# Kernel tuning notes

Hardware: AMD Instinct MI355X
Metric: run time of the kernel (lower is better)

Reference implementation:

```python
import jax, jax.numpy as jnp
import numpy as np

H, D, DIM = 8, 128, 1024   # heads, dim_head, model dim (inner_dim = H*D = DIM)
QB, N = 16, 512            # 'q' and 'n' dims of the [q, n, dim] inputs


def layer_norm(x, g, b, eps=1e-5):
    mu = x.mean(-1, keepdims=True)
    var = ((x - mu) ** 2).mean(-1, keepdims=True)
    return (x - mu) / jnp.sqrt(var + eps) * g + b


def setup_inputs() -> dict:
    key = jax.random.key(0)
    ks = jax.random.split(key, 8)
    rn = lambda k, shape, s=1.0: jax.random.normal(k, shape, jnp.float32) * s
    return {
        'q': rn(ks[0], (QB, N, DIM)),
        'k': rn(ks[1], (QB, N, DIM)),
        'v': rn(ks[2], (QB, N, DIM)),
        'ln_g': jnp.ones(DIM, jnp.float32),
        'ln_b': jnp.zeros(DIM, jnp.float32),
        'w_in': rn(ks[3], (H * D, DIM), 0.02),          # Linear(dim -> inner_dim), no bias
        'wp_w1': rn(ks[4], (D, 2 * D), 0.05),           # weight_predictor Linear(2d -> d)
        'wp_b1': jnp.zeros(D, jnp.float32),
        'wp_ln_g': jnp.ones(D, jnp.float32),
        'wp_ln_b': jnp.zeros(D, jnp.float32),
        'wp_w2': rn(ks[5], (3, D), 0.05),               # Linear(d -> 3)
        'wp_b2': jnp.zeros(3, jnp.float32),
        'w_out': rn(ks[6], (DIM, H * D), 0.02),         # output Linear(inner_dim -> dim)
        'b_out': jnp.zeros(DIM, jnp.float32),
    }


def reference(q, k, v, ln_g, ln_b, w_in, wp_w1, wp_b1, wp_ln_g, wp_ln_b,
              wp_w2, wp_b2, w_out, b_out):
    def proj(t):
        x = layer_norm(t, ln_g, ln_b) @ w_in.T                 # [Q, N, H*D]
        Qd, Nd = t.shape[0], t.shape[1]
        return x.reshape(Qd, Nd, H, D).transpose(2, 0, 1, 3)   # [h, q, n, d]

    f_q, f_k, f_v = proj(q), proj(k), proj(v)

    # cosine similarity component
    dots = jnp.einsum('hqnd,hqmd->hqnm', f_q, f_k)
    qn = jnp.linalg.norm(f_q, axis=-1)                          # [h, q, n]
    kn = jnp.linalg.norm(f_k, axis=-1)                          # [h, q, m]
    cosine_sim = dots / (qn[..., :, None] * kn[..., None, :])

    q_centered = f_q - f_q.mean(-1, keepdims=True)

    # variance component (unbiased variance, clipped ratio vs target_var=1)
    q_var = jnp.var(f_q, axis=-1, ddof=1)
    k_var = jnp.var(f_k, axis=-1, ddof=1)
    q_ratio = 2.0 * jnp.minimum(q_var, 1.0) / (q_var + 1.0)
    k_ratio = 2.0 * jnp.minimum(k_var, 1.0) / (k_var + 1.0)
    var_component = jnp.einsum('hqn,hqm->hqnm', q_ratio, k_ratio)

    # decorrelation-scaled covariance component (overwrites the dead loop in the source)
    q_flat = q_centered.reshape(H, -1, D)                        # [h, q*n, d]
    feat_corr = jnp.einsum('hnd,hne->hde', q_flat, q_flat) / q_flat.shape[1]
    feat_corr = feat_corr * (1.0 - jnp.eye(D, dtype=feat_corr.dtype))
    decorr_score = jnp.linalg.norm(feat_corr, axis=(-2, -1)) / (D * D)
    decorr_scale = jnp.exp(-5.0 * decorr_score)[:, None, None, None]
    cov_component = cosine_sim * decorr_scale

    # dynamic per-head weight mixing
    q_global = f_q.mean(axis=(1, 2))                             # [h, d]
    k_global = f_k.mean(axis=(1, 2))
    feats = jnp.concatenate([q_global, k_global], axis=-1)       # [h, 2d]
    h1 = jnp.maximum(layer_norm(feats @ wp_w1.T + wp_b1, wp_ln_g, wp_ln_b), 0.0)
    weights = jax.nn.softmax(h1 @ wp_w2.T + wp_b2, axis=-1)      # [h, 3]
    cw = weights[:, 0][:, None, None, None]
    vw = weights[:, 1][:, None, None, None]
    ww = weights[:, 2][:, None, None, None]
    mixed = cw * cosine_sim + vw * cov_component + ww * var_component

    out = jnp.einsum('hqnm,hqmd->hqnd', mixed, f_v)
    out = out.transpose(1, 2, 0, 3).reshape(q.shape[0], q.shape[1], H * D)
    return out @ w_out.T + b_out
```

## Files before the change

### kernel.cpp

```cpp
#include <hip/hip_runtime.h>
#include <hip/hip_bf16.h>

typedef unsigned short u16;
typedef __attribute__((ext_vector_type(8))) short short8;
typedef __attribute__((ext_vector_type(4))) float floatx4;

#define H 8
#define D 128
#define DIM 1024
#define QB 16
#define NSEQ 512
#define R 8192

__device__ inline u16 f2b(float x) {
    union { float f; unsigned int u; } c{x};
    unsigned int lsb = (c.u >> 16) & 1;
    unsigned int r = c.u + 0x7fffu + lsb;
    return (u16)(r >> 16);
}
__device__ inline float b2f(u16 u) {
    union { unsigned int i; float f; } c;
    c.i = (unsigned int)u << 16;
    return c.f;
}

#define GLOAD_LDS16(gptr, lptr)                                                        \
    __builtin_amdgcn_global_load_lds(                                                  \
        (const __attribute__((address_space(1))) unsigned int*)(gptr),                 \
        (__attribute__((address_space(3))) unsigned int*)(lptr), 16, 0, 0)

__global__ __launch_bounds__(256) void ln_all(const float* __restrict__ q,
                                              const float* __restrict__ k,
                                              const float* __restrict__ v,
                                              const float* __restrict__ g,
                                              const float* __restrict__ b,
                                              u16* __restrict__ out) {
    const float* src = (blockIdx.y == 0) ? q : (blockIdx.y == 1) ? k : v;
    int r = blockIdx.x;
    int tid = threadIdx.x;
    const int wv = tid >> 6, lane = tid & 63;
    const float* row = src + (size_t)r * DIM;
    float4 vv = *(const float4*)(row + tid * 4);
    float sum = vv.x + vv.y + vv.z + vv.w;
    float sq = vv.x * vv.x + vv.y * vv.y + vv.z * vv.z + vv.w * vv.w;
#pragma unroll
    for (int o = 32; o > 0; o >>= 1) {
        sum += __shfl_xor(sum, o);
        sq  += __shfl_xor(sq, o);
    }
    __shared__ float s1[4], s2[4];
    if (lane == 0) { s1[wv] = sum; s2[wv] = sq; }
    __syncthreads();
    sum = s1[0] + s1[1] + s1[2] + s1[3];
    sq  = s2[0] + s2[1] + s2[2] + s2[3];
    float mean = sum * (1.0f / DIM);
    float var = sq * (1.0f / DIM) - mean * mean;
    float rstd = rsqrtf(var + 1e-5f);
    float4 gv = *(const float4*)(g + tid * 4);
    float4 bv = *(const float4*)(b + tid * 4);
    ushort4 pk;
    pk.x = f2b((vv.x - mean) * rstd * gv.x + bv.x);
    pk.y = f2b((vv.y - mean) * rstd * gv.y + bv.y);
    pk.z = f2b((vv.z - mean) * rstd * gv.z + bv.z);
    pk.w = f2b((vv.w - mean) * rstd * gv.w + bv.w);
    *(ushort4*)(out + ((size_t)blockIdx.y * R + r) * DIM + tid * 4) = pk;
}

__global__ __launch_bounds__(256) void cvt2_kernel(const float* __restrict__ a,
                                                   const float* __restrict__ b,
                                                   u16* __restrict__ oa,
                                                   u16* __restrict__ ob, int n4each) {
    int i = blockIdx.x * 256 + threadIdx.x;
    const float* src; u16* dst; int j;
    if (i < n4each) { src = a; dst = oa; j = i; }
    else            { src = b; dst = ob; j = i - n4each; }
    float4 v = *(const float4*)(src + (size_t)j * 4);
    ushort4 pk;
    pk.x = f2b(v.x); pk.y = f2b(v.y); pk.z = f2b(v.z); pk.w = f2b(v.w);
    *(ushort4*)(dst + (size_t)j * 4) = pk;
}

__global__ __launch_bounds__(256) void gemm_qkv(const u16* __restrict__ A,
                                                const u16* __restrict__ B,
                                                u16* __restrict__ qT,
                                                u16* __restrict__ fqb,
                                                u16* __restrict__ kTh,
                                                u16* __restrict__ vT,
                                                float* __restrict__ qn,
                                                float* __restrict__ qm,
                                                float* __restrict__ qr,
                                                float* __restrict__ kn,
                                                float* __restrict__ kr) {
    __shared__ u16 smem[19712];
    u16* As  = smem;
    u16* Bs  = smem + 4096;
    u16* As2 = smem + 8192;
    u16* Bs2 = smem + 12288;
    float* sred = (float*)(smem + 18432);
    float* invb = (float*)(smem + 19456);

    const int tid = threadIdx.x;
    const int bb = blockIdx.x;
    const int xcd = bb & 7, j0 = bb >> 3;
    const int h = j0 & 7;
    const int rowblk = xcd * 24 + (j0 >> 3);
    const int m0 = rowblk * 128, n0 = h * 128;
    const int seg = rowblk >> 6;
    const int lrb = (rowblk & 63) * 128;

    const int wave = tid >> 6, lane = tid & 63;
    const int wm = (wave >> 1) * 64, wn = (wave & 1) * 64;
    const int fr = lane & 15, kq = lane >> 4;
    const int srow = tid >> 2, scol = (tid & 3) * 8;

    floatx4 acc[4][4] = {};
    const size_t aOff0 = (size_t)(m0 + srow) * DIM + scol;
    const size_t aOff1 = (size_t)(m0 + 64 + srow) * DIM + scol;
    const size_t bOff0 = (size_t)(n0 + srow) * DIM + scol;
    const size_t bOff1 = (size_t)(n0 + 64 + srow) * DIM + scol;

    for (int kt = 0; kt < DIM; kt += 64) {
        GLOAD_LDS16(A + aOff0 + kt, As + tid * 8);
        GLOAD_LDS16(A + aOff1 + kt, As + (256 + tid) * 8);
        GLOAD_LDS16(B + bOff0 + kt, Bs + tid * 8);
        GLOAD_LDS16(B + bOff1 + kt, Bs + (256 + tid) * 8);
        GLOAD_LDS16(A + aOff0 + kt + 32, As2 + tid * 8);
        GLOAD_LDS16(A + aOff1 + kt + 32, As2 + (256 + tid) * 8);
        GLOAD_LDS16(B + bOff0 + kt + 32, Bs2 + tid * 8);
        GLOAD_LDS16(B + bOff1 + kt + 32, Bs2 + (256 + tid) * 8);
        __syncthreads();
        short8 xf[4], wf[4];
#pragma unroll
        for (int i = 0; i < 4; i++)
            xf[i] = *(const short8*)&As[(wm + i * 16 + fr) * 32 + kq * 8];
#pragma unroll
        for (int j = 0; j < 4; j++)
            wf[j] = *(const short8*)&Bs[(wn + j * 16 + fr) * 32 + kq * 8];
#pragma unroll
        for (int j = 0; j < 4; j++)
#pragma unroll
            for (int i = 0; i < 4; i++)
                acc[j][i] = __builtin_amdgcn_mfma_f32_16x16x32_bf16(wf[j], xf[i], acc[j][i], 0, 0, 0);
        short8 xg[4], wg[4];
#pragma unroll
        for (int i = 0; i < 4; i++)
            xg[i] = *(const short8*)&As2[(wm + i * 16 + fr) * 32 + kq * 8];
#pragma unroll
        for (int j = 0; j < 4; j++)
            wg[j] = *(const short8*)&Bs2[(wn + j * 16 + fr) * 32 + kq * 8];
#pragma unroll
        for (int j = 0; j < 4; j++)
#pragma unroll
            for (int i = 0; i < 4; i++)
                acc[j][i] = __builtin_amdgcn_mfma_f32_16x16x32_bf16(wg[j], xg[i], acc[j][i], 0, 0, 0);
        __syncthreads();
    }

    if (seg <= 1) {
        const int half = wn >> 6;
#pragma unroll
        for (int i = 0; i < 4; i++) {
            float s = 0.0f, qs = 0.0f;
#pragma unroll
            for (int j = 0; j < 4; j++)
#pragma unroll
                for (int rg = 0; rg < 4; rg++) {
                    float vv = acc[j][i][rg];
                    s += vv; qs += vv * vv;
                }
            s += __shfl_xor(s, 16); qs += __shfl_xor(qs, 16);
            s += __shfl_xor(s, 32); qs += __shfl_xor(qs, 32);
            if (kq == 0) {
                int rl = wm + i * 16 + fr;
                sred[rl * 4 + half * 2 + 0] = s;
                sred[rl * 4 + half * 2 + 1] = qs;
            }
        }
        __syncthreads();
        if (tid < 128) {
            float sum = sred[tid * 4 + 0] + sred[tid * 4 + 2];
            float sq  = sred[tid * 4 + 1] + sred[tid * 4 + 3];
            float nrm = sqrtf(sq);
            float var = (sq - sum * sum * (1.0f / D)) * (1.0f / (D - 1));
            float ratio = 2.0f * fminf(var, 1.0f) / (var + 1.0f);
            size_t idx = (size_t)h * R + lrb + tid;
            if (seg == 0) {
                qn[idx] = nrm; qm[idx] = sum * (1.0f / D); qr[idx] = ratio;
            } else {
                kn[idx] = nrm; kr[idx] = ratio;
                invb[tid] = 1.0f / nrm;
            }
        }
        __syncthreads();
    }

    u16* dstT = (seg == 0) ? qT : (seg == 1) ? kTh : vT;
#pragma unroll
    for (int i = 0; i < 4; i++) {
        const int rl = wm + i * 16 + fr;
        const float sc = (seg == 1) ? invb[rl] : 1.0f;
#pragma unroll
        for (int j = 0; j < 4; j++) {
#pragma unroll
            for (int rg = 0; rg < 4; rg++) {
                const int cl = wn + j * 16 + kq * 4 + rg;
                dstT[(size_t)(h * D + cl) * R + lrb + rl] = f2b(acc[j][i][rg] * sc);
            }
        }
    }

    if (seg == 0) {
        __syncthreads();
        u16* Tw = smem + wave * 4608;
#pragma unroll
        for (int i = 0; i < 4; i++)
#pragma unroll
            for (int j = 0; j < 4; j++) {
                ushort4 pk;
                pk.x = f2b(acc[j][i][0]); pk.y = f2b(acc[j][i][1]);
                pk.z = f2b(acc[j][i][2]); pk.w = f2b(acc[j][i][3]);
                *(ushort4*)&Tw[(i * 16 + fr) * 72 + j * 16 + kq * 4] = pk;
            }
        __syncthreads();
#pragma unroll
        for (int p = 0; p < 16; p++) {
            int rloc = p * 4 + kq;
            int c4 = fr * 4;
            ushort4 v = *(const ushort4*)&Tw[rloc * 72 + c4];
            *(ushort4*)&fqb[(size_t)(lrb + wm + rloc) * DIM + h * D + wn + c4] = v;
        }
    }
}

__global__ __launch_bounds__(256) void colsum2(const u16* __restrict__ qT,
                                               const u16* __restrict__ kTh,
                                               const float* __restrict__ qm,
                                               const float* __restrict__ kn,
                                               float* __restrict__ qg,
                                               float* __restrict__ kg,
                                               float* __restrict__ ubuf,
                                               float* __restrict__ s2) {
    int dg = blockIdx.x, h = blockIdx.y, mode = blockIdx.z, tid = threadIdx.x;
    const u16* fT = mode ? kTh : qT;
    const float* wvec = mode ? kn : qm;
    const int wv = tid >> 6, lane = tid & 63;
    __shared__ float red[2][4];
    const float* wp = wvec + (size_t)h * R;
    for (int dd = 0; dd < 8; dd++) {
        int d = dg * 8 + dd;
        const u16* rowp = fT + (size_t)(h * D + d) * R;
        float s = 0.0f, su = 0.0f;
        for (int it = 0; it < 8; it++) {
            int r = it * 1024 + tid * 4;
            uint2 pv = *(const uint2*)(rowp + r);
            float4 w = *(const float4*)(wp + r);
            float v0 = b2f((u16)(pv.x & 0xffffu)), v1 = b2f((u16)(pv.x >> 16));
            float v2 = b2f((u16)(pv.y & 0xffffu)), v3 = b2f((u16)(pv.y >> 16));
            if (mode) s += v0 * w.x + v1 * w.y + v2 * w.z + v3 * w.w;
            else {
                s += v0 + v1 + v2 + v3;
                su += v0 * w.x + v1 * w.y + v2 * w.z + v3 * w.w;
            }
        }
#pragma unroll
        for (int o = 32; o > 0; o >>= 1) {
            s += __shfl_xor(s, o);
            su += __shfl_xor(su, o);
        }
        if (lane == 0) { red[0][wv] = s; red[1][wv] = su; }
        __syncthreads();
        if (tid == 0) {
            float S  = red[0][0] + red[0][1] + red[0][2] + red[0][3];
            float SU = red[1][0] + red[1][1] + red[1][2] + red[1][3];
            if (mode) kg[h * D + d] = S * (1.0f / R);
            else { qg[h * D + d] = S * (1.0f / R); ubuf[h * D + d] = SU; }
        }
        __syncthreads();
    }
    if (!mode && dg == 0) {
        float t = 0.0f;
        for (int it = 0; it < 8; it++) {
            float4 m4 = *(const float4*)(qm + (size_t)h * R + it * 1024 + tid * 4);
            t += m4.x * m4.x + m4.y * m4.y + m4.z * m4.z + m4.w * m4.w;
        }
#pragma unroll
        for (int o = 32; o > 0; o >>= 1) t += __shfl_xor(t, o);
        if (lane == 0) red[0][wv] = t;
        __syncthreads();
        if (tid == 0) s2[h] = red[0][0] + red[0][1] + red[0][2] + red[0][3];
    }
}

__global__ __launch_bounds__(256) void syrk_q(const u16* __restrict__ qT,
                                              float* __restrict__ P) {
    __shared__ u16 As[128 * 32];
    const int c = blockIdx.x, h = blockIdx.y;
    const int tid = threadIdx.x;
    const int wave = tid >> 6, lane = tid & 63;
    const int wm = (wave >> 1) * 64, wn = (wave & 1) * 64;
    const int fr = lane & 15, kq = lane >> 4;
    const int srow = tid >> 2, scol = (tid & 3) * 8;
    floatx4 acc[4][4] = {};
    const size_t a0 = (size_t)(h * D + srow) * R + c * 256 + scol;
    const size_t a1 = (size_t)(h * D + 64 + srow) * R + c * 256 + scol;
    for (int kt = 0; kt < 256; kt += 32) {
        GLOAD_LDS16(qT + a0 + kt, As + tid * 8);
        GLOAD_LDS16(qT + a1 + kt, As + (256 + tid) * 8);
        __syncthreads();
        short8 af[4], bf[4];
#pragma unroll
        for (int i = 0; i < 4; i++)
            af[i] = *(const short8*)&As[(wm + i * 16 + fr) * 32 + kq * 8];
#pragma unroll
        for (int j = 0; j < 4; j++)
            bf[j] = *(const short8*)&As[(wn + j * 16 + fr) * 32 + kq * 8];
#pragma unroll
        for (int i = 0; i < 4; i++)
#pragma unroll
            for (int j = 0; j < 4; j++)
                acc[i][j] = __builtin_amdgcn_mfma_f32_16x16x32_bf16(af[i], bf[j], acc[i][j], 0, 0, 0);
        __syncthreads();
    }
    float* base = P + (size_t)(h * 32 + c) * (D * D);
#pragma unroll
    for (int i = 0; i < 4; i++) {
        int dr = wm + i * 16 + kq * 4;
#pragma unroll
        for (int j = 0; j < 4; j++) {
            int ec = wn + j * 16 + fr;
#pragma unroll
            for (int r = 0; r < 4; r++)
                base[(size_t)(dr + r) * D + ec] = acc[i][j][r];
        }
    }
}

__global__ __launch_bounds__(256) void decorr_sum(const float* __restrict__ P,
                                                  const float* __restrict__ ubuf,
                                                  const float* __restrict__ s2b,
                                                  float* __restrict__ Spart) {
    int bx = blockIdx.x, h = blockIdx.y, tid = threadIdx.x;
    float s2h = s2b[h];
    float S = 0.0f;
    for (int t = 0; t < 2; t++) {
        int de = bx * 512 + t * 256 + tid;
        int dd = de >> 7, ee = de & 127;
        float g = 0.0f;
        for (int c = 0; c < 32; c++)
            g += P[(size_t)(h * 32 + c) * (D * D) + de];
        if (dd != ee) {
            float vv = (g - ubuf[h * D + dd] - ubuf[h * D + ee] + s2h) * (1.0f / R);
            S += vv * vv;
        }
    }
#pragma unroll
    for (int o = 32; o > 0; o >>= 1) S += __shfl_xor(S, o);
    __shared__ float r1[4];
    if ((tid & 63) == 0) r1[tid >> 6] = S;
    __syncthreads();
    if (tid == 0) Spart[h * 32 + bx] = r1[0] + r1[1] + r1[2] + r1[3];
}

__global__ __launch_bounds__(256) void head_kernel(const float* __restrict__ Spart,
                                                   const float* __restrict__ qg,
                                                   const float* __restrict__ kg,
                                                   const float* __restrict__ w1,
                                                   const float* __restrict__ b1,
                                                   const float* __restrict__ lng,
                                                   const float* __restrict__ lnb,
                                                   const float* __restrict__ w2,
                                                   const float* __restrict__ b2,
                                                   float* __restrict__ coef) {
    int h = blockIdx.x, tid = threadIdx.x;
    __shared__ float s1[256], s2[256], s3[256];
    __shared__ float feats[256];
    float Ssum = 0.0f;
    for (int c = 0; c < 32; c++) Ssum += Spart[h * 32 + c];
    float dscale = expf(-5.0f * sqrtf(Ssum) / (float)(D * D));
    feats[tid] = (tid < 128) ? qg[h * D + tid] : kg[h * D + tid - 128];
    __syncthreads();
    float yv = 0.0f;
    if (tid < 128) {
        float a = b1[tid];
        for (int i = 0; i < 256; i++) a = fmaf(feats[i], w1[tid * 256 + i], a);
        yv = a;
    }
    s1[tid] = (tid < 128) ? yv : 0.0f;
    s2[tid] = (tid < 128) ? yv * yv : 0.0f;
    __syncthreads();
    for (int s = 128; s > 0; s >>= 1) {
        if (tid < s) { s1[tid] += s1[tid + s]; s2[tid] += s2[tid + s]; }
        __syncthreads();
    }
    float mean = s1[0] * (1.0f / 128.0f);
    float var = s2[0] * (1.0f / 128.0f) - mean * mean;
    float rstd = rsqrtf(var + 1e-5f);
    float rel = 0.0f;
    if (tid < 128)
        rel = fmaxf((yv - mean) * rstd * lng[tid] + lnb[tid], 0.0f);
    __syncthreads();
    s1[tid] = (tid < 128) ? rel * w2[0 * 128 + tid] : 0.0f;
    s2[tid] = (tid < 128) ? rel * w2[1 * 128 + tid] : 0.0f;
    s3[tid] = (tid < 128) ? rel * w2[2 * 128 + tid] : 0.0f;
    __syncthreads();
    for (int s = 128; s > 0; s >>= 1) {
        if (tid < s) { s1[tid] += s1[tid + s]; s2[tid] += s2[tid + s]; s3[tid] += s3[tid + s]; }
        __syncthreads();
    }
    if (tid == 0) {
        float g0 = s1[0] + b2[0], g1 = s2[0] + b2[1], g2 = s3[0] + b2[2];
        float mx = fmaxf(g0, fmaxf(g1, g2));
        float e0 = expf(g0 - mx), e1 = expf(g1 - mx), e2 = expf(g2 - mx);
        float inv = 1.0f / (e0 + e1 + e2);
        coef[h * 2 + 0] = e0 * inv + e1 * inv * dscale;
        coef[h * 2 + 1] = e2 * inv;
    }
}

__global__ __launch_bounds__(256) void ktv_mfma(const u16* __restrict__ kTh,
                                                const u16* __restrict__ vT,
                                                const float* __restrict__ kr,
                                                u16* __restrict__ Mt,
                                                float* __restrict__ sv) {
    __shared__ u16 As[128 * 32];
    __shared__ u16 Bs[128 * 32];
    __shared__ float wbuf[32];
    __shared__ float svred[256];
    const int qi = blockIdx.x, h = blockIdx.y;
    const int tid = threadIdx.x;
    const int wave = tid >> 6, lane = tid & 63;
    const int wm = (wave >> 1) * 64, wn = (wave & 1) * 64;
    const int fr = lane & 15, kq = lane >> 4;
    const int srow = tid >> 2, scol = (tid & 3) * 8;
    const int m0g = qi * 512;
    const size_t a0 = (size_t)(h * D + srow) * R + m0g + scol;
    const size_t a1 = (size_t)(h * D + 64 + srow) * R + m0g + scol;
    const int e_id = tid & 127, eh = tid >> 7, mb16 = (tid >> 7) * 16;
    float svacc = 0.0f;
    floatx4 acc[4][4] = {};
    for (int kt = 0; kt < 512; kt += 32) {
        GLOAD_LDS16(vT + a0 + kt, As + tid * 8);
        GLOAD_LDS16(vT + a1 + kt, As + (256 + tid) * 8);
        GLOAD_LDS16(kTh + a0 + kt, Bs + tid * 8);
        GLOAD_LDS16(kTh + a1 + kt, Bs + (256 + tid) * 8);
        if (tid < 32) wbuf[tid] = kr[(size_t)h * R + m0g + kt + tid];
        __syncthreads();
        short8 af[4], bf[4];
#pragma unroll
        for (int i = 0; i < 4; i++)
            af[i] = *(const short8*)&As[(wm + i * 16 + fr) * 32 + kq * 8];
#pragma unroll
        for (int j = 0; j < 4; j++)
            bf[j] = *(const short8*)&Bs[(wn + j * 16 + fr) * 32 + kq * 8];
#pragma unroll
        for (int i = 0; i < 4; i++)
#pragma unroll
            for (int j = 0; j < 4; j++)
                acc[i][j] = __builtin_amdgcn_mfma_f32_16x16x32_bf16(af[i], bf[j], acc[i][j], 0, 0, 0);
        {
            short8 va = *(const short8*)&As[e_id * 32 + mb16];
            short8 vb = *(const short8*)&As[e_id * 32 + mb16 + 8];
#pragma unroll
            for (int jm = 0; jm < 8; jm++)
                svacc += b2f((u16)va[jm]) * wbuf[mb16 + jm];
#pragma unroll
            for (int jm = 0; jm < 8; jm++)
                svacc += b2f((u16)vb[jm]) * wbuf[mb16 + 8 + jm];
        }
        __syncthreads();
    }
    (void)eh;
    u16* mb = Mt + (size_t)(h * QB + qi) * D * D;
#pragma unroll
    for (int i = 0; i < 4; i++) {
        int er = wm + i * 16 + kq * 4;
#pragma unroll
        for (int j = 0; j < 4; j++) {
            int dc = wn + j * 16 + fr;
#pragma unroll
            for (int r = 0; r < 4; r++)
                mb[(size_t)(er + r) * D + dc] = f2b(acc[i][j][r]);
        }
    }
    svred[tid] = svacc;
    __syncthreads();
    if (tid < 128)
        sv[(size_t)(h * QB + qi) * D + tid] = svred[tid] + svred[tid + 128];
}

__global__ __launch_bounds__(256) void attn_mfma(const u16* __restrict__ fqb,
                                                 const u16* __restrict__ Mt,
                                                 const float* __restrict__ qn,
                                                 const float* __restrict__ qr,
                                                 const float* __restrict__ sv,
                                                 const float* __restrict__ coef,
                                                 u16* __restrict__ outb) {
    __shared__ u16 As[128 * 32];
    __shared__ u16 Bs[128 * 32];
    const int nb = blockIdx.x, qi = blockIdx.y, h = blockIdx.z;
    const int tid = threadIdx.x;
    const int wave = tid >> 6, lane = tid & 63;
    const int wm = (wave >> 1) * 64, wn = (wave & 1) * 64;
    const int fr = lane & 15, kq = lane >> 4;
    const int srow = tid >> 2, scol = (tid & 3) * 8;
    const int n0g = qi * 512 + nb * 128;
    const size_t a0 = (size_t)(n0g + srow) * DIM + h * D + scol;
    const size_t a1 = (size_t)(n0g + 64 + srow) * DIM + h * D + scol;
    const u16* mtb = Mt + (size_t)(h * QB + qi) * D * D;
    floatx4 acc[4][4] = {};
    for (int kt = 0; kt < 128; kt += 32) {
        GLOAD_LDS16(fqb + a0 + kt, As + tid * 8);
        GLOAD_LDS16(fqb + a1 + kt, As + (256 + tid) * 8);
        GLOAD_LDS16(mtb + (size_t)srow * D + kt + scol, Bs + tid * 8);
        GLOAD_LDS16(mtb + (size_t)(64 + srow) * D + kt + scol, Bs + (256 + tid) * 8);
        __syncthreads();
        short8 af[4], bf[4];
#pragma unroll
        for (int i = 0; i < 4; i++)
            af[i] = *(const short8*)&As[(wm + i * 16 + fr) * 32 + kq * 8];
#pragma unroll
        for (int j = 0; j < 4; j++)
            bf[j] = *(const short8*)&Bs[(wn + j * 16 + fr) * 32 + kq * 8];
#pragma unroll
        for (int i = 0; i < 4; i++)
#pragma unroll
            for (int j = 0; j < 4; j++)
                acc[i][j] = __builtin_amdgcn_mfma_f32_16x16x32_bf16(af[i], bf[j], acc[i][j], 0, 0, 0);
        __syncthreads();
    }
    float c0 = coef[2 * h], c1 = coef[2 * h + 1];
#pragma unroll
    for (int i = 0; i < 4; i++) {
        int nr = n0g + wm + i * 16 + kq * 4;
        float4 nv = *(const float4*)&qn[(size_t)h * R + nr];
        float4 rv = *(const float4*)&qr[(size_t)h * R + nr];
        float sc1[4] = {c0 / nv.x, c0 / nv.y, c0 / nv.z, c0 / nv.w};
        float sc2[4] = {c1 * rv.x, c1 * rv.y, c1 * rv.z, c1 * rv.w};
#pragma unroll
        for (int j = 0; j < 4; j++) {
            int ec = wn + j * 16 + fr;
            float svv = sv[(size_t)(h * QB + qi) * D + ec];
#pragma unroll
            for (int r = 0; r < 4; r++)
                outb[(size_t)(nr + r) * DIM + h * D + ec] = f2b(sc1[r] * acc[i][j][r] + sc2[r] * svv);
        }
    }
}

__global__ __launch_bounds__(256) void gemm_out(const u16* __restrict__ A,
                                                const u16* __restrict__ B,
                                                const float* __restrict__ bias,
                                                float* __restrict__ C) {
    __shared__ u16 As[128 * 64];
    __shared__ u16 Bs[128 * 64];
    const int tid = threadIdx.x;
    const int bb = blockIdx.x;
    const int xcd = bb & 7, jj = bb >> 3;
    const int col = jj & 7, rowblk = xcd * 8 + (jj >> 3);
    const int m0 = rowblk * 128, n0 = col * 128;
    const int wave = tid >> 6, lane = tid & 63;
    const int wm = (wave >> 1) * 64, wn = (wave & 1) * 64;
    const int fr = lane & 15, kq = lane >> 4;
    const int srow = tid >> 2, scol = (tid & 3) * 8;
    floatx4 acc[4][4] = {};
    const size_t aOff0 = (size_t)(m0 + srow) * DIM + scol;
    const size_t aOff1 = (size_t)(m0 + 64 + srow) * DIM + scol;
    const size_t bOff0 = (size_t)(n0 + srow) * DIM + scol;
    const size_t bOff1 = (size_t)(n0 + 64 + srow) * DIM + scol;
    for (int kt = 0; kt < DIM; kt += 64) {
        GLOAD_LDS16(A + aOff0 + kt, As + tid * 8);
        GLOAD_LDS16(A + aOff1 + kt, As + (256 + tid) * 8);
        GLOAD_LDS16(A + aOff0 + kt + 32, As + (512 + tid) * 8);
        GLOAD_LDS16(A + aOff1 + kt + 32, As + (768 + tid) * 8);
        GLOAD_LDS16(B + bOff0 + kt, Bs + tid * 8);
        GLOAD_LDS16(B + bOff1 + kt, Bs + (256 + tid) * 8);
        GLOAD_LDS16(B + bOff0 + kt + 32, Bs + (512 + tid) * 8);
        GLOAD_LDS16(B + bOff1 + kt + 32, Bs + (768 + tid) * 8);
        __syncthreads();
        short8 af[4], bf[4];
#pragma unroll
        for (int i = 0; i < 4; i++)
            af[i] = *(const short8*)&As[(wm + i * 16 + fr) * 32 + kq * 8];
#pragma unroll
        for (int j = 0; j < 4; j++)
            bf[j] = *(const short8*)&Bs[(wn + j * 16 + fr) * 32 + kq * 8];
#pragma unroll
        for (int i = 0; i < 4; i++)
#pragma unroll
            for (int j = 0; j < 4; j++)
                acc[i][j] = __builtin_amdgcn_mfma_f32_16x16x32_bf16(af[i], bf[j], acc[i][j], 0, 0, 0);
        short8 ag[4], bg[4];
#pragma unroll
        for (int i = 0; i < 4; i++)
            ag[i] = *(const short8*)&As[4096 + (wm + i * 16 + fr) * 32 + kq * 8];
#pragma unroll
        for (int j = 0; j < 4; j++)
            bg[j] = *(const short8*)&Bs[4096 + (wn + j * 16 + fr) * 32 + kq * 8];
#pragma unroll
        for (int i = 0; i < 4; i++)
#pragma unroll
            for (int j = 0; j < 4; j++)
                acc[i][j] = __builtin_amdgcn_mfma_f32_16x16x32_bf16(ag[i], bg[j], acc[i][j], 0, 0, 0);
        __syncthreads();
    }
#pragma unroll
    for (int i = 0; i < 4; i++) {
        int rbase = m0 + wm + i * 16 + kq * 4;
#pragma unroll
        for (int j = 0; j < 4; j++) {
            int c = n0 + wn + j * 16 + fr;
            float badd = bias[c];
#pragma unroll
            for (int r = 0; r < 4; r++)
                C[(size_t)(rbase + r) * DIM + c] = acc[i][j][r] + badd;
        }
    }
}

extern "C" void kernel_launch(void* const* d_in, const int* in_sizes, int n_in,
                              void* d_out, int out_size, void* d_ws, size_t ws_size,
                              hipStream_t stream) {
    (void)in_sizes; (void)n_in; (void)out_size; (void)ws_size;
    const float* q      = (const float*)d_in[0];
    const float* k      = (const float*)d_in[1];
    const float* v      = (const float*)d_in[2];
    const float* ln_g   = (const float*)d_in[3];
    const float* ln_b   = (const float*)d_in[4];
    const float* w_in   = (const float*)d_in[5];
    const float* wp_w1  = (const float*)d_in[6];
    const float* wp_b1  = (const float*)d_in[7];
    const float* wp_lng = (const float*)d_in[8];
    const float* wp_lnb = (const float*)d_in[9];
    const float* wp_w2  = (const float*)d_in[10];
    const float* wp_b2  = (const float*)d_in[11];
    const float* w_out  = (const float*)d_in[12];
    const float* b_out  = (const float*)d_in[13];
    float* out = (float*)d_out;

    constexpr size_t F = (size_t)R * DIM;
    u16* lnall   = (u16*)d_ws;
    u16* fqb     = lnall + 3 * F;
    u16* qT      = fqb + F;
    u16* kTh     = qT + F;
    u16* vT      = kTh + F;
    u16* w_in16  = vT + F;
    u16* w_out16 = w_in16 + (size_t)DIM * DIM;
    u16* Mt      = w_out16 + (size_t)DIM * DIM;
    float* P     = (float*)(Mt + (size_t)H * QB * D * D);
    float* qn    = P + (size_t)32 * H * D * D;
    float* qm    = qn + (size_t)H * R;
    float* qr    = qm + (size_t)H * R;
    float* kn    = qr + (size_t)H * R;
    float* kr    = kn + (size_t)H * R;
    float* qg    = kr + (size_t)H * R;
    float* kg    = qg + H * D;
    float* ubuf  = kg + H * D;
    float* s2    = ubuf + H * D;
    float* Spart = s2 + H;
    float* coef  = Spart + H * 8;
    float* svb   = coef + 16;
    float* SpartN = qm;

    cvt2_kernel<<<2048, 256, 0, stream>>>(w_in, w_out, w_in16, w_out16, DIM * DIM / 4);
    ln_all<<<dim3(R, 3), 256, 0, stream>>>(q, k, v, ln_g, ln_b, lnall);

    gemm_qkv<<<1536, 256, 0, stream>>>(lnall, w_in16, qT, fqb, kTh, vT,
                                       qn, qm, qr, kn, kr);

    colsum2<<<dim3(16, H, 2), 256, 0, stream>>>(qT, kTh, qm, kn, qg, kg, ubuf, s2);

    syrk_q<<<dim3(32, H), 256, 0, stream>>>(qT, P);
    decorr_sum<<<dim3(32, H), 256, 0, stream>>>(P, ubuf, s2, SpartN);

    head_kernel<<<H, 256, 0, stream>>>(SpartN, qg, kg, wp_w1, wp_b1,
                                       wp_lng, wp_lnb, wp_w2, wp_b2, coef);

    ktv_mfma<<<dim3(QB, H), 256, 0, stream>>>(kTh, vT, kr, Mt, svb);

    attn_mfma<<<dim3(4, QB, H), 256, 0, stream>>>(fqb, Mt, qn, qr, svb, coef, lnall);

    gemm_out<<<512, 256, 0, stream>>>(lnall, w_out16, b_out, out);
}
```

Before: 338.4 us.

## Merge independent kernels into fused launches and stage transposed stores through LDS

Merges the weight conversion and layernorm kernels into one launch, and merges colsum, syrk and ktv into a single 'fanout' kernel whose block ranges do different jobs. The three were separate launches that each left the GPU underfilled. The transposed qT/kT/vT epilogue in gemm_qkv now goes through shared memory so the global writes are 16-byte vectors instead of scattered 2-byte stores. The P partials are written as float4 with a transposed index, which relies on the block being symmetric. Mixing heterogeneous blocks can unbalance the schedule, since the ktv blocks are longer than the others.

```diff
diff --git a/kernel.cpp b/kernel.cpp
--- a/kernel.cpp
+++ b/kernel.cpp
@@ -29,15 +29,34 @@
         (const __attribute__((address_space(1))) unsigned int*)(gptr),                 \
         (__attribute__((address_space(3))) unsigned int*)(lptr), 16, 0, 0)
 
-__global__ __launch_bounds__(256) void ln_all(const float* __restrict__ q,
-                                              const float* __restrict__ k,
-                                              const float* __restrict__ v,
-                                              const float* __restrict__ g,
-                                              const float* __restrict__ b,
-                                              u16* __restrict__ out) {
-    const float* src = (blockIdx.y == 0) ? q : (blockIdx.y == 1) ? k : v;
-    int r = blockIdx.x;
-    int tid = threadIdx.x;
+__global__ __launch_bounds__(256) void prep(const float* __restrict__ q,
+                                            const float* __restrict__ k,
+                                            const float* __restrict__ v,
+                                            const float* __restrict__ g,
+                                            const float* __restrict__ b,
+                                            u16* __restrict__ out,
+                                            const float* __restrict__ w_in,
+                                            const float* __restrict__ w_out,
+                                            u16* __restrict__ w_in16,
+                                            u16* __restrict__ w_out16) {
+    const int bb = blockIdx.x;
+    const int tid = threadIdx.x;
+    if (bb < 2048) {
+        const int n4each = DIM * DIM / 4;
+        int i = bb * 256 + tid;
+        const float* src; u16* dst; int j;
+        if (i < n4each) { src = w_in;  dst = w_in16;  j = i; }
+        else            { src = w_out; dst = w_out16; j = i - n4each; }
+        float4 vv = *(const float4*)(src + (size_t)j * 4);
+        ushort4 pk;
+        pk.x = f2b(vv.x); pk.y = f2b(vv.y); pk.z = f2b(vv.z); pk.w = f2b(vv.w);
+        *(ushort4*)(dst + (size_t)j * 4) = pk;
+        return;
+    }
+    const int b2 = bb - 2048;
+    const int y = b2 >> 13;
+    const int r = b2 & 8191;
+    const float* src = (y == 0) ? q : (y == 1) ? k : v;
     const int wv = tid >> 6, lane = tid & 63;
     const float* row = src + (size_t)r * DIM;
     float4 vv = *(const float4*)(row + tid * 4);
@@ -63,21 +82,7 @@
     pk.y = f2b((vv.y - mean) * rstd * gv.y + bv.y);
     pk.z = f2b((vv.z - mean) * rstd * gv.z + bv.z);
     pk.w = f2b((vv.w - mean) * rstd * gv.w + bv.w);
-    *(ushort4*)(out + ((size_t)blockIdx.y * R + r) * DIM + tid * 4) = pk;
-}
-
-__global__ __launch_bounds__(256) void cvt2_kernel(const float* __restrict__ a,
-                                                   const float* __restrict__ b,
-                                                   u16* __restrict__ oa,
-                                                   u16* __restrict__ ob, int n4each) {
-    int i = blockIdx.x * 256 + threadIdx.x;
-    const float* src; u16* dst; int j;
-    if (i < n4each) { src = a; dst = oa; j = i; }
-    else            { src = b; dst = ob; j = i - n4each; }
-    float4 v = *(const float4*)(src + (size_t)j * 4);
-    ushort4 pk;
-    pk.x = f2b(v.x); pk.y = f2b(v.y); pk.z = f2b(v.z); pk.w = f2b(v.w);
-    *(ushort4*)(dst + (size_t)j * 4) = pk;
+    *(ushort4*)(out + ((size_t)y * R + r) * DIM + tid * 4) = pk;
 }
 
 __global__ __launch_bounds__(256) void gemm_qkv(const u16* __restrict__ A,
@@ -91,7 +96,7 @@
                                                 float* __restrict__ qr,
                                                 float* __restrict__ kn,
                                                 float* __restrict__ kr) {
-    __shared__ u16 smem[19712];
+    __shared__ __align__(16) u16 smem[19712];
     u16* As  = smem;
     u16* Bs  = smem + 4096;
     u16* As2 = smem + 8192;
@@ -204,8 +209,17 @@
 #pragma unroll
             for (int rg = 0; rg < 4; rg++) {
                 const int cl = wn + j * 16 + kq * 4 + rg;
-                dstT[(size_t)(h * D + cl) * R + lrb + rl] = f2b(acc[j][i][rg] * sc);
-            }
+                smem[cl * 136 + rl] = f2b(acc[j][i][rg] * sc);
+            }
+        }
+    }
+    __syncthreads();
+    {
+        const int c = tid >> 1, hf = tid & 1;
+#pragma unroll
+        for (int p = 0; p < 8; p++) {
+            short8 w = *(const short8*)&smem[c * 136 + hf * 64 + p * 8];
+            *(short8*)&dstT[(size_t)(h * D + c) * R + lrb + hf * 64 + p * 8] = w;
         }
     }
 
@@ -232,105 +246,175 @@
     }
 }
 
-__global__ __launch_bounds__(256) void colsum2(const u16* __restrict__ qT,
-                                               const u16* __restrict__ kTh,
-                                               const float* __restrict__ qm,
-                                               const float* __restrict__ kn,
-                                               float* __restrict__ qg,
-                                               float* __restrict__ kg,
-                                               float* __restrict__ ubuf,
-                                               float* __restrict__ s2) {
-    int dg = blockIdx.x, h = blockIdx.y, mode = blockIdx.z, tid = threadIdx.x;
-    const u16* fT = mode ? kTh : qT;
-    const float* wvec = mode ? kn : qm;
-    const int wv = tid >> 6, lane = tid & 63;
-    __shared__ float red[2][4];
-    const float* wp = wvec + (size_t)h * R;
-    for (int dd = 0; dd < 8; dd++) {
-        int d = dg * 8 + dd;
-        const u16* rowp = fT + (size_t)(h * D + d) * R;
-        float s = 0.0f, su = 0.0f;
-        for (int it = 0; it < 8; it++) {
-            int r = it * 1024 + tid * 4;
-            uint2 pv = *(const uint2*)(rowp + r);
-            float4 w = *(const float4*)(wp + r);
-            float v0 = b2f((u16)(pv.x & 0xffffu)), v1 = b2f((u16)(pv.x >> 16));
-            float v2 = b2f((u16)(pv.y & 0xffffu)), v3 = b2f((u16)(pv.y >> 16));
-            if (mode) s += v0 * w.x + v1 * w.y + v2 * w.z + v3 * w.w;
-            else {
-                s += v0 + v1 + v2 + v3;
-                su += v0 * w.x + v1 * w.y + v2 * w.z + v3 * w.w;
-            }
-        }
-#pragma unroll
-        for (int o = 32; o > 0; o >>= 1) {
-            s += __shfl_xor(s, o);
-            su += __shfl_xor(su, o);
-        }
-        if (lane == 0) { red[0][wv] = s; red[1][wv] = su; }
-        __syncthreads();
-        if (tid == 0) {
-            float S  = red[0][0] + red[0][1] + red[0][2] + red[0][3];
-            float SU = red[1][0] + red[1][1] + red[1][2] + red[1][3];
-            if (mode) kg[h * D + d] = S * (1.0f / R);
-            else { qg[h * D + d] = S * (1.0f / R); ubuf[h * D + d] = SU; }
-        }
-        __syncthreads();
-    }
-    if (!mode && dg == 0) {
-        float t = 0.0f;
-        for (int it = 0; it < 8; it++) {
-            float4 m4 = *(const float4*)(qm + (size_t)h * R + it * 1024 + tid * 4);
-            t += m4.x * m4.x + m4.y * m4.y + m4.z * m4.z + m4.w * m4.w;
-        }
-#pragma unroll
-        for (int o = 32; o > 0; o >>= 1) t += __shfl_xor(t, o);
-        if (lane == 0) red[0][wv] = t;
-        __syncthreads();
-        if (tid == 0) s2[h] = red[0][0] + red[0][1] + red[0][2] + red[0][3];
-    }
-}
-
-__global__ __launch_bounds__(256) void syrk_q(const u16* __restrict__ qT,
-                                              float* __restrict__ P) {
-    __shared__ u16 As[128 * 32];
-    const int c = blockIdx.x, h = blockIdx.y;
+__global__ __launch_bounds__(256) void fanout(const u16* __restrict__ qT,
+                                              const u16* __restrict__ kTh,
+                                              const u16* __restrict__ vT,
+                                              const float* __restrict__ qm,
+                                              const float* __restrict__ kn,
+                                              const float* __restrict__ kr,
+                                              float* __restrict__ qg,
+                                              float* __restrict__ kg,
+                                              float* __restrict__ ubuf,
+                                              float* __restrict__ s2,
+                                              float* __restrict__ P,
+                                              u16* __restrict__ Mt,
+                                              float* __restrict__ sv) {
+    __shared__ __align__(16) u16 sm[8832];
+    u16* As = sm;
+    u16* Bs = sm + 4096;
+    float* wbuf  = (float*)(sm + 8192);
+    float* svred = (float*)(sm + 8256);
+    float* redS  = (float*)(sm + 8768);
+
+    const int bb = blockIdx.x;
     const int tid = threadIdx.x;
     const int wave = tid >> 6, lane = tid & 63;
     const int wm = (wave >> 1) * 64, wn = (wave & 1) * 64;
     const int fr = lane & 15, kq = lane >> 4;
     const int srow = tid >> 2, scol = (tid & 3) * 8;
-    floatx4 acc[4][4] = {};
-    const size_t a0 = (size_t)(h * D + srow) * R + c * 256 + scol;
-    const size_t a1 = (size_t)(h * D + 64 + srow) * R + c * 256 + scol;
-    for (int kt = 0; kt < 256; kt += 32) {
-        GLOAD_LDS16(qT + a0 + kt, As + tid * 8);
-        GLOAD_LDS16(qT + a1 + kt, As + (256 + tid) * 8);
-        __syncthreads();
-        short8 af[4], bf[4];
-#pragma unroll
-        for (int i = 0; i < 4; i++)
-            af[i] = *(const short8*)&As[(wm + i * 16 + fr) * 32 + kq * 8];
-#pragma unroll
-        for (int j = 0; j < 4; j++)
-            bf[j] = *(const short8*)&As[(wn + j * 16 + fr) * 32 + kq * 8];
-#pragma unroll
-        for (int i = 0; i < 4; i++)
+
+    if (bb < 128) {
+        const int qi = bb & 15, h = bb >> 4;
+        const int m0g = qi * 512;
+        const size_t a0 = (size_t)(h * D + srow) * R + m0g + scol;
+        const size_t a1 = (size_t)(h * D + 64 + srow) * R + m0g + scol;
+        const int e_id = tid & 127, mb16 = (tid >> 7) * 16;
+        float svacc = 0.0f;
+        floatx4 acc[4][4] = {};
+        for (int kt = 0; kt < 512; kt += 32) {
+            GLOAD_LDS16(vT + a0 + kt, As + tid * 8);
+            GLOAD_LDS16(vT + a1 + kt, As + (256 + tid) * 8);
+            GLOAD_LDS16(kTh + a0 + kt, Bs + tid * 8);
+            GLOAD_LDS16(kTh + a1 + kt, Bs + (256 + tid) * 8);
+            if (tid < 32) wbuf[tid] = kr[(size_t)h * R + m0g + kt + tid];
+            __syncthreads();
+            short8 af[4], bf[4];
+#pragma unroll
+            for (int i = 0; i < 4; i++)
+                af[i] = *(const short8*)&As[(wm + i * 16 + fr) * 32 + kq * 8];
 #pragma unroll
             for (int j = 0; j < 4; j++)
-                acc[i][j] = __builtin_amdgcn_mfma_f32_16x16x32_bf16(af[i], bf[j], acc[i][j], 0, 0, 0);
-        __syncthreads();
-    }
-    float* base = P + (size_t)(h * 32 + c) * (D * D);
-#pragma unroll
-    for (int i = 0; i < 4; i++) {
-        int dr = wm + i * 16 + kq * 4;
-#pragma unroll
-        for (int j = 0; j < 4; j++) {
-            int ec = wn + j * 16 + fr;
-#pragma unroll
-            for (int r = 0; r < 4; r++)
-                base[(size_t)(dr + r) * D + ec] = acc[i][j][r];
+                bf[j] = *(const short8*)&Bs[(wn + j * 16 + fr) * 32 + kq * 8];
+#pragma unroll
+            for (int i = 0; i < 4; i++)
+#pragma unroll
+                for (int j = 0; j < 4; j++)
+                    acc[i][j] = __builtin_amdgcn_mfma_f32_16x16x32_bf16(af[i], bf[j], acc[i][j], 0, 0, 0);
+            {
+                short8 va = *(const short8*)&As[e_id * 32 + mb16];
+                short8 vb = *(const short8*)&As[e_id * 32 + mb16 + 8];
+#pragma unroll
+                for (int jm = 0; jm < 8; jm++)
+                    svacc += b2f((u16)va[jm]) * wbuf[mb16 + jm];
+#pragma unroll
+                for (int jm = 0; jm < 8; jm++)
+                    svacc += b2f((u16)vb[jm]) * wbuf[mb16 + 8 + jm];
+            }
+            __syncthreads();
+        }
+        u16* mb = Mt + (size_t)(h * QB + qi) * D * D;
+#pragma unroll
+        for (int i = 0; i < 4; i++) {
+            int er = wm + i * 16 + kq * 4;
+#pragma unroll
+            for (int j = 0; j < 4; j++) {
+                int dc = wn + j * 16 + fr;
+#pragma unroll
+                for (int r = 0; r < 4; r++)
+                    mb[(size_t)(er + r) * D + dc] = f2b(acc[i][j][r]);
+            }
+        }
+        svred[tid] = svacc;
+        __syncthreads();
+        if (tid < 128)
+            sv[(size_t)(h * QB + qi) * D + tid] = svred[tid] + svred[tid + 128];
+    } else if (bb < 384) {
+        const int t = bb - 128;
+        const int c = t & 31, h = t >> 5;
+        floatx4 acc[4][4] = {};
+        const size_t a0 = (size_t)(h * D + srow) * R + c * 256 + scol;
+        const size_t a1 = (size_t)(h * D + 64 + srow) * R + c * 256 + scol;
+        for (int kt = 0; kt < 256; kt += 32) {
+            GLOAD_LDS16(qT + a0 + kt, As + tid * 8);
+            GLOAD_LDS16(qT + a1 + kt, As + (256 + tid) * 8);
+            __syncthreads();
+            short8 af[4], bf[4];
+#pragma unroll
+            for (int i = 0; i < 4; i++)
+                af[i] = *(const short8*)&As[(wm + i * 16 + fr) * 32 + kq * 8];
+#pragma unroll
+            for (int j = 0; j < 4; j++)
+                bf[j] = *(const short8*)&As[(wn + j * 16 + fr) * 32 + kq * 8];
+#pragma unroll
+            for (int i = 0; i < 4; i++)
+#pragma unroll
+                for (int j = 0; j < 4; j++)
+                    acc[i][j] = __builtin_amdgcn_mfma_f32_16x16x32_bf16(af[i], bf[j], acc[i][j], 0, 0, 0);
+            __syncthreads();
+        }
+        float* base = P + (size_t)(h * 32 + c) * (D * D);
+#pragma unroll
+        for (int i = 0; i < 4; i++) {
+            int dr = wm + i * 16 + kq * 4;
+#pragma unroll
+            for (int j = 0; j < 4; j++) {
+                int ec = wn + j * 16 + fr;
+                float4 f4;
+                f4.x = acc[i][j][0]; f4.y = acc[i][j][1];
+                f4.z = acc[i][j][2]; f4.w = acc[i][j][3];
+                *(float4*)&base[(size_t)ec * D + dr] = f4;
+            }
+        }
+    } else {
+        const int t = bb - 384;
+        const int dg = t & 15, h = (t >> 4) & 7, mode = t >> 7;
+        const u16* fT = mode ? kTh : qT;
+        const float* wvec = mode ? kn : qm;
+        const int wv = tid >> 6;
+        float (*red)[4] = (float(*)[4])redS;
+        const float* wp = wvec + (size_t)h * R;
+        for (int dd = 0; dd < 8; dd++) {
+            int d = dg * 8 + dd;
+            const u16* rowp = fT + (size_t)(h * D + d) * R;
+            float s = 0.0f, su = 0.0f;
+            for (int it = 0; it < 8; it++) {
+                int r = it * 1024 + tid * 4;
+                uint2 pv = *(const uint2*)(rowp + r);
+                float4 w = *(const float4*)(wp + r);
+                float v0 = b2f((u16)(pv.x & 0xffffu)), v1 = b2f((u16)(pv.x >> 16));
+                float v2 = b2f((u16)(pv.y & 0xffffu)), v3 = b2f((u16)(pv.y >> 16));
+                if (mode) s += v0 * w.x + v1 * w.y + v2 * w.z + v3 * w.w;
+                else {
+                    s += v0 + v1 + v2 + v3;
+                    su += v0 * w.x + v1 * w.y + v2 * w.z + v3 * w.w;
+                }
+            }
+#pragma unroll
+            for (int o = 32; o > 0; o >>= 1) {
+                s += __shfl_xor(s, o);
+                su += __shfl_xor(su, o);
+            }
+            if ((tid & 63) == 0) { red[0][wv] = s; red[1][wv] = su; }
+            __syncthreads();
+            if (tid == 0) {
+                float S  = red[0][0] + red[0][1] + red[0][2] + red[0][3];
+                float SU = red[1][0] + red[1][1] + red[1][2] + red[1][3];
+                if (mode) kg[h * D + d] = S * (1.0f / R);
+                else { qg[h * D + d] = S * (1.0f / R); ubuf[h * D + d] = SU; }
+            }
+            __syncthreads();
+        }
+        if (!mode && dg == 0) {
+            float tt = 0.0f;
+            for (int it = 0; it < 8; it++) {
+                float4 m4 = *(const float4*)(qm + (size_t)h * R + it * 1024 + tid * 4);
+                tt += m4.x * m4.x + m4.y * m4.y + m4.z * m4.z + m4.w * m4.w;
+            }
+#pragma unroll
+            for (int o = 32; o > 0; o >>= 1) tt += __shfl_xor(tt, o);
+            if ((tid & 63) == 0) red[0][wv] = tt;
+            __syncthreads();
+            if (tid == 0) s2[h] = red[0][0] + red[0][1] + red[0][2] + red[0][3];
         }
     }
 }
@@ -415,77 +499,6 @@
         coef[h * 2 + 0] = e0 * inv + e1 * inv * dscale;
         coef[h * 2 + 1] = e2 * inv;
     }
-}
-
-__global__ __launch_bounds__(256) void ktv_mfma(const u16* __restrict__ kTh,
-                                                const u16* __restrict__ vT,
-                                                const float* __restrict__ kr,
-                                                u16* __restrict__ Mt,
-                                                float* __restrict__ sv) {
-    __shared__ u16 As[128 * 32];
-    __shared__ u16 Bs[128 * 32];
-    __shared__ float wbuf[32];
-    __shared__ float svred[256];
-    const int qi = blockIdx.x, h = blockIdx.y;
-    const int tid = threadIdx.x;
-    const int wave = tid >> 6, lane = tid & 63;
-    const int wm = (wave >> 1) * 64, wn = (wave & 1) * 64;
-    const int fr = lane & 15, kq = lane >> 4;
-    const int srow = tid >> 2, scol = (tid & 3) * 8;
-    const int m0g = qi * 512;
-    const size_t a0 = (size_t)(h * D + srow) * R + m0g + scol;
-    const size_t a1 = (size_t)(h * D + 64 + srow) * R + m0g + scol;
-    const int e_id = tid & 127, eh = tid >> 7, mb16 = (tid >> 7) * 16;
-    float svacc = 0.0f;
-    floatx4 acc[4][4] = {};
-    for (int kt = 0; kt < 512; kt += 32) {
-        GLOAD_LDS16(vT + a0 + kt, As + tid * 8);
-        GLOAD_LDS16(vT + a1 + kt, As + (256 + tid) * 8);
-        GLOAD_LDS16(kTh + a0 + kt, Bs + tid * 8);
-        GLOAD_LDS16(kTh + a1 + kt, Bs + (256 + tid) * 8);
-        if (tid < 32) wbuf[tid] = kr[(size_t)h * R + m0g + kt + tid];
-        __syncthreads();
-        short8 af[4], bf[4];
-#pragma unroll
-        for (int i = 0; i < 4; i++)
-            af[i] = *(const short8*)&As[(wm + i * 16 + fr) * 32 + kq * 8];
-#pragma unroll
-        for (int j = 0; j < 4; j++)
-            bf[j] = *(const short8*)&Bs[(wn + j * 16 + fr) * 32 + kq * 8];
-#pragma unroll
-        for (int i = 0; i < 4; i++)
-#pragma unroll
-            for (int j = 0; j < 4; j++)
-                acc[i][j] = __builtin_amdgcn_mfma_f32_16x16x32_bf16(af[i], bf[j], acc[i][j], 0, 0, 0);
-        {
-            short8 va = *(const short8*)&As[e_id * 32 + mb16];
-            short8 vb = *(const short8*)&As[e_id * 32 + mb16 + 8];
-#pragma unroll
-            for (int jm = 0; jm < 8; jm++)
-                svacc += b2f((u16)va[jm]) * wbuf[mb16 + jm];
-#pragma unroll
-            for (int jm = 0; jm < 8; jm++)
-                svacc += b2f((u16)vb[jm]) * wbuf[mb16 + 8 + jm];
-        }
-        __syncthreads();
-    }
-    (void)eh;
-    u16* mb = Mt + (size_t)(h * QB + qi) * D * D;
-#pragma unroll
-    for (int i = 0; i < 4; i++) {
-        int er = wm + i * 16 + kq * 4;
-#pragma unroll
-        for (int j = 0; j < 4; j++) {
-            int dc = wn + j * 16 + fr;
-#pragma unroll
-            for (int r = 0; r < 4; r++)
-                mb[(size_t)(er + r) * D + dc] = f2b(acc[i][j][r]);
-        }
-    }
-    svred[tid] = svacc;
-    __syncthreads();
-    if (tid < 128)
-        sv[(size_t)(h * QB + qi) * D + tid] = svred[tid] + svred[tid + 128];
 }
 
 __global__ __launch_bounds__(256) void attn_mfma(const u16* __restrict__ fqb,
@@ -661,22 +674,20 @@
     float* svb   = coef + 16;
     float* SpartN = qm;
 
-    cvt2_kernel<<<2048, 256, 0, stream>>>(w_in, w_out, w_in16, w_out16, DIM * DIM / 4);
-    ln_all<<<dim3(R, 3), 256, 0, stream>>>(q, k, v, ln_g, ln_b, lnall);
+    prep<<<26624, 256, 0, stream>>>(q, k, v, ln_g, ln_b, lnall,
+                                    w_in, w_out, w_in16, w_out16);
 
     gemm_qkv<<<1536, 256, 0, stream>>>(lnall, w_in16, qT, fqb, kTh, vT,
                                        qn, qm, qr, kn, kr);
 
-    colsum2<<<dim3(16, H, 2), 256, 0, stream>>>(qT, kTh, qm, kn, qg, kg, ubuf, s2);
-
-    syrk_q<<<dim3(32, H), 256, 0, stream>>>(qT, P);
+    fanout<<<640, 256, 0, stream>>>(qT, kTh, vT, qm, kn, kr,
+                                    qg, kg, ubuf, s2, P, Mt, svb);
+
     decorr_sum<<<dim3(32, H), 256, 0, stream>>>(P, ubuf, s2, SpartN);
 
     head_kernel<<<H, 256, 0, stream>>>(SpartN, qg, kg, wp_w1, wp_b1,
                                        wp_lng, wp_lnb, wp_w2, wp_b2, coef);
 
-    ktv_mfma<<<dim3(QB, H), 256, 0, stream>>>(kTh, vT, kr, Mt, svb);
-
     attn_mfma<<<dim3(4, QB, H), 256, 0, stream>>>(fqb, Mt, qn, qr, svb, coef, lnall);
 
     gemm_out<<<512, 256, 0, stream>>>(lnall, w_out16, b_out, out);
```

Measured after the change: 328.7 us. 2.9% less time.
